# Kernel tuning notes

Measured on AMD Instinct MI355X. Metric: run time of the kernel, lower is better.

The kernel has to match this reference:

```python
import jax, jax.numpy as jnp
import numpy as np

N_NODES = 75000
N_EDGES = 1200000


def gcn_conv(x, src, dst, W, b, n):
    # linear transform first (PyG GCNConv applies lin before propagate)
    h = x @ W  # [n, out]
    # add self loops
    loop = jnp.arange(n, dtype=src.dtype)
    s = jnp.concatenate([src, loop])
    d = jnp.concatenate([dst, loop])
    # symmetric normalization: deg computed on destination after self-loops
    deg = jnp.zeros((n,), dtype=h.dtype).at[d].add(1.0)
    dinv = jnp.where(deg > 0, jax.lax.rsqrt(deg), 0.0)
    norm = dinv[s] * dinv[d]  # [E+n]
    msgs = h[s] * norm[:, None]  # gather + scale, [E+n, out]
    out = jax.ops.segment_sum(msgs, d, num_segments=n)  # scatter-add
    return out + b


def setup_inputs() -> dict:
    key = jax.random.key(0)
    ks = jax.random.split(key, 6)
    x = jax.random.normal(ks[0], (N_NODES, 64), dtype=jnp.float32)
    edge_index = jax.random.randint(ks[1], (2, N_EDGES), 0, N_NODES, dtype=jnp.int64)
    # Glorot-ish scaled weights
    W1 = jax.random.normal(ks[2], (64, 64), dtype=jnp.float32) * (1.0 / np.sqrt(64))
    b1 = jax.random.normal(ks[3], (64,), dtype=jnp.float32) * 0.01
    W2 = jax.random.normal(ks[4], (64, 16), dtype=jnp.float32) * (1.0 / np.sqrt(64))
    b2 = jax.random.normal(ks[5], (16,), dtype=jnp.float32) * 0.01
    return {"x": x, "edge_index": edge_index, "W1": W1, "b1": b1, "W2": W2, "b2": b2}


def reference(x, edge_index, W1, b1, W2, b2):
    src, dst = edge_index[0], edge_index[1]
    h = gcn_conv(x, src, dst, W1, b1, N_NODES)
    h = jax.nn.relu(h)
    # dropout is identity in eval mode
    out = gcn_conv(h, src, dst, W2, b2, N_NODES)
    return out
```

## Files before the change

kernel.cpp:

```cpp
#include <hip/hip_runtime.h>


#define NBSHIFT 9
#define BUCKET_NODES 512
#define CAP 10240
#define CHA 8192
#define TA 512
#define TB 512
#define MAXNB 160
#define EPT 16

__device__ __forceinline__ unsigned bfpack(float a, float b) {
  unsigned ua = __float_as_uint(a), ub = __float_as_uint(b);
  ua += 0x7fffu + ((ua >> 16) & 1u);
  ub += 0x7fffu + ((ub >> 16) & 1u);
  return (ua >> 16) | (ub & 0xffff0000u);
}
__device__ __forceinline__ float bflo(unsigned u) { return __uint_as_float(u << 16); }
__device__ __forceinline__ float bfhi(unsigned u) { return __uint_as_float(u & 0xffff0000u); }

__launch_bounds__(TA)
__global__ void kA_bucket(const int* __restrict__ src, const int* __restrict__ dst,
                          int* __restrict__ bucketCur, int* __restrict__ bucketArr,
                          int NB, int E) {
  __shared__ int stage[CHA];
  __shared__ unsigned char binOf[CHA];
  __shared__ int cnt[MAXNB];
  __shared__ int off[MAXNB];
  __shared__ int gpos[MAXNB];
  __shared__ int cursor[MAXNB];
  __shared__ int scanbuf[256];
  int t = threadIdx.x;
  int e0 = blockIdx.x * CHA;

  for (int i = t; i < NB; i += TA) cnt[i] = 0;
  __syncthreads();
  int dreg[EPT];
  #pragma unroll
  for (int j = 0; j < EPT; j++) {
    int e = e0 + t + j * TA;
    dreg[j] = (e < E) ? dst[e] : -1;
    if (dreg[j] >= 0) atomicAdd(&cnt[dreg[j] >> NBSHIFT], 1);
  }
  __syncthreads();
  if (t < 256) scanbuf[t] = (t < NB) ? cnt[t] : 0;
  __syncthreads();
  for (int o = 1; o < 256; o <<= 1) {
    int add = (t < 256 && t >= o) ? scanbuf[t - o] : 0;
    __syncthreads();
    if (t < 256) scanbuf[t] += add;
    __syncthreads();
  }
  if (t < NB) {
    off[t] = scanbuf[t] - cnt[t];
    cursor[t] = off[t];
    gpos[t] = (cnt[t] > 0) ? atomicAdd(&bucketCur[t], cnt[t]) : 0;
  }
  __syncthreads();
  #pragma unroll
  for (int j = 0; j < EPT; j++) {
    int e = e0 + t + j * TA;
    if (dreg[j] >= 0) {
      int d = dreg[j], s = src[e];
      int b = d >> NBSHIFT;
      int p = atomicAdd(&cursor[b], 1);
      stage[p] = (s << NBSHIFT) | (d & (BUCKET_NODES - 1));
      binOf[p] = (unsigned char)b;
    }
  }
  __syncthreads();
  int total = scanbuf[255];
  for (int i = t; i < total; i += TA) {
    int b = binOf[i];
    int destIdx = gpos[b] + (i - off[b]);
    if (destIdx < CAP) bucketArr[b * CAP + destIdx] = stage[i];
  }
}

__launch_bounds__(TB)
__global__ void kB_fill(const int* __restrict__ bucketArr, const int* __restrict__ bucketCur,
                        int* __restrict__ rp, float* __restrict__ dinv,
                        int* __restrict__ col, int N, int NB) {
  __shared__ int cnts[MAXNB];
  __shared__ int hist[BUCKET_NODES];
  __shared__ int cur[BUCKET_NODES];
  __shared__ int wsum[8], woff[8];
  __shared__ int s_base;
  int b = blockIdx.x;
  int t = threadIdx.x;
  int nE = min(bucketCur[b], CAP);
  int base = b * CAP;

  if (t < NB) cnts[t] = min(bucketCur[t], CAP);
  hist[t] = 0;
  __syncthreads();
  for (int i = t; i < nE; i += TB)
    atomicAdd(&hist[bucketArr[base + i] & (BUCKET_NODES - 1)], 1);
  __syncthreads();
  int myv = hist[t];
  int lane = t & 63, w = t >> 6;
  int incl = myv;
  #pragma unroll
  for (int o = 1; o < 64; o <<= 1) {
    int v = __shfl_up(incl, o);
    if (lane >= o) incl += v;
  }
  if (lane == 63) wsum[w] = incl;
  __syncthreads();
  if (t == 0) {
    int acc = 0;
    for (int i = 0; i < b; i++) acc += cnts[i];
    s_base = acc;
    int a2 = 0;
    #pragma unroll
    for (int i = 0; i < 8; i++) { woff[i] = a2; a2 += wsum[i]; }
    if (b == NB - 1) rp[N] = acc + nE;
  }
  __syncthreads();
  int gexcl = s_base + woff[w] + (incl - myv);
  cur[t] = gexcl;
  int gnode = b * BUCKET_NODES + t;
  if (gnode < N) {
    rp[gnode] = gexcl;
    dinv[gnode] = rsqrtf((float)(myv + 1));
  }
  __syncthreads();
  for (int i = t; i < nE; i += TB) {
    int v = bucketArr[base + i];
    int p = atomicAdd(&cur[v & (BUCKET_NODES - 1)], 1);
    col[p] = v >> NBSHIFT;
  }
}

__launch_bounds__(256)
__global__ void k_gemm64(const float4* __restrict__ X4, const float4* __restrict__ W4,
                         const float* __restrict__ dinv, uint2* __restrict__ outb,
                         int n) {
  __shared__ float4 Xs[64 * 17];
  __shared__ float4 Ws[64 * 16];
  int t = threadIdx.x;
  int base = blockIdx.x * 64;
  {
    int rr = t >> 2, q = t & 3;
    int r = base + rr;
    #pragma unroll
    for (int c = 0; c < 4; c++) {
      float4 v = make_float4(0.f, 0.f, 0.f, 0.f);
      if (r < n) v = X4[r * 16 + q * 4 + c];
      Xs[rr * 17 + q * 4 + c] = v;
      Ws[t + 256 * c] = W4[t + 256 * c];
    }
  }
  __syncthreads();

  int tx = t & 15, ty = t >> 4;
  float4 a0 = make_float4(0.f, 0.f, 0.f, 0.f), a1 = a0, a2 = a0, a3 = a0;
  #pragma unroll
  for (int kb = 0; kb < 16; kb++) {
    float4 x0 = Xs[(ty * 4 + 0) * 17 + kb];
    float4 x1 = Xs[(ty * 4 + 1) * 17 + kb];
    float4 x2 = Xs[(ty * 4 + 2) * 17 + kb];
    float4 x3 = Xs[(ty * 4 + 3) * 17 + kb];
    float4 w0 = Ws[(kb * 4 + 0) * 16 + tx];
    float4 w1 = Ws[(kb * 4 + 1) * 16 + tx];
    float4 w2 = Ws[(kb * 4 + 2) * 16 + tx];
    float4 w3 = Ws[(kb * 4 + 3) * 16 + tx];
    #define FMA4(A, XS) \
      A.x = fmaf(XS.x, w0.x, A.x); A.y = fmaf(XS.x, w0.y, A.y); \
      A.z = fmaf(XS.x, w0.z, A.z); A.w = fmaf(XS.x, w0.w, A.w); \
      A.x = fmaf(XS.y, w1.x, A.x); A.y = fmaf(XS.y, w1.y, A.y); \
      A.z = fmaf(XS.y, w1.z, A.z); A.w = fmaf(XS.y, w1.w, A.w); \
      A.x = fmaf(XS.z, w2.x, A.x); A.y = fmaf(XS.z, w2.y, A.y); \
      A.z = fmaf(XS.z, w2.z, A.z); A.w = fmaf(XS.z, w2.w, A.w); \
      A.x = fmaf(XS.w, w3.x, A.x); A.y = fmaf(XS.w, w3.y, A.y); \
      A.z = fmaf(XS.w, w3.z, A.z); A.w = fmaf(XS.w, w3.w, A.w);
    FMA4(a0, x0) FMA4(a1, x1) FMA4(a2, x2) FMA4(a3, x3)
    #undef FMA4
  }
  #pragma unroll
  for (int i = 0; i < 4; i++) {
    int r = base + ty * 4 + i;
    if (r < n) {
      float s = dinv[r];
      float4 a = (i == 0) ? a0 : (i == 1) ? a1 : (i == 2) ? a2 : a3;
      uint2 pk;
      pk.x = bfpack(a.x * s, a.y * s);
      pk.y = bfpack(a.z * s, a.w * s);
      outb[r * 16 + tx] = pk;
    }
  }
}

__launch_bounds__(256)
__global__ void k_aggW2(const uint2* __restrict__ hsb,
                        const int* __restrict__ rp,
                        const int* __restrict__ col,
                        const float* __restrict__ dinv,
                        const float* __restrict__ b1,
                        const float* __restrict__ W2,
                        unsigned* __restrict__ hs2b,
                        int n) {
  __shared__ float W2s[1024];
  for (int i = threadIdx.x; i < 1024; i += 256) W2s[i] = W2[i];
  __syncthreads();
  int lane = threadIdx.x & 63;
  int c = lane & 15;
  int node = ((blockIdx.x * blockDim.x + threadIdx.x) >> 6) * 4 + (lane >> 4);
  if (node >= n) return;

  float4 b14 = ((const float4*)b1)[c];
  int s0 = rp[node], s1 = rp[node + 1];
  int dt = s1 - s0 + 1;
  float ax = 0.f, ay = 0.f, az = 0.f, aw = 0.f;
  int t = 0;
  int i0 = node, i1 = 0, i2 = 0, i3 = 0, i4 = 0, i5 = 0, i6 = 0, i7 = 0;
  if (1 < dt) i1 = col[s0 + 0];
  if (2 < dt) i2 = col[s0 + 1];
  if (3 < dt) i3 = col[s0 + 2];
  if (4 < dt) i4 = col[s0 + 3];
  if (5 < dt) i5 = col[s0 + 4];
  if (6 < dt) i6 = col[s0 + 5];
  if (7 < dt) i7 = col[s0 + 6];
  while (t < dt) {
    int c0 = i0, c1 = i1, c2 = i2, c3 = i3, c4 = i4, c5 = i5, c6 = i6, c7 = i7;
    bool h1_ = (t + 1) < dt, h2_ = (t + 2) < dt, h3_ = (t + 3) < dt;
    bool h4_ = (t + 4) < dt, h5_ = (t + 5) < dt, h6_ = (t + 6) < dt;
    bool h7_ = (t + 7) < dt;
    int tn = t + 8;
    if (tn + 0 < dt) i0 = col[s0 + tn - 1];
    if (tn + 1 < dt) i1 = col[s0 + tn + 0];
    if (tn + 2 < dt) i2 = col[s0 + tn + 1];
    if (tn + 3 < dt) i3 = col[s0 + tn + 2];
    if (tn + 4 < dt) i4 = col[s0 + tn + 3];
    if (tn + 5 < dt) i5 = col[s0 + tn + 4];
    if (tn + 6 < dt) i6 = col[s0 + tn + 5];
    if (tn + 7 < dt) i7 = col[s0 + tn + 6];
    uint2 u0 = hsb[c0 * 16 + c];
    uint2 u1 = h1_ ? hsb[c1 * 16 + c] : make_uint2(0u, 0u);
    uint2 u2 = h2_ ? hsb[c2 * 16 + c] : make_uint2(0u, 0u);
    uint2 u3 = h3_ ? hsb[c3 * 16 + c] : make_uint2(0u, 0u);
    uint2 u4 = h4_ ? hsb[c4 * 16 + c] : make_uint2(0u, 0u);
    uint2 u5 = h5_ ? hsb[c5 * 16 + c] : make_uint2(0u, 0u);
    uint2 u6 = h6_ ? hsb[c6 * 16 + c] : make_uint2(0u, 0u);
    uint2 u7 = h7_ ? hsb[c7 * 16 + c] : make_uint2(0u, 0u);
    #define ACC(U) \
      ax += bflo(U.x); ay += bfhi(U.x); az += bflo(U.y); aw += bfhi(U.y);
    ACC(u0) ACC(u1) ACC(u2) ACC(u3) ACC(u4) ACC(u5) ACC(u6) ACC(u7)
    #undef ACC
    t = tn;
  }
  float dv = dinv[node];
  float h0  = fmaxf(ax * dv + b14.x, 0.f);
  float h1v = fmaxf(ay * dv + b14.y, 0.f);
  float h2v = fmaxf(az * dv + b14.z, 0.f);
  float h3v = fmaxf(aw * dv + b14.w, 0.f);

  float val = 0.f;
  int gb = lane & 48;
  #pragma unroll
  for (int kq = 0; kq < 16; kq++) {
    int srcl = gb + kq;
    float v0 = __shfl(h0, srcl);
    float v1 = __shfl(h1v, srcl);
    float v2 = __shfl(h2v, srcl);
    float v3 = __shfl(h3v, srcl);
    val = fmaf(v0, W2s[(4 * kq + 0) * 16 + c], val);
    val = fmaf(v1, W2s[(4 * kq + 1) * 16 + c], val);
    val = fmaf(v2, W2s[(4 * kq + 2) * 16 + c], val);
    val = fmaf(v3, W2s[(4 * kq + 3) * 16 + c], val);
  }
  val *= dv;
  float vnext = __shfl_down(val, 1);
  if ((c & 1) == 0) hs2b[node * 8 + (c >> 1)] = bfpack(val, vnext);
}

__launch_bounds__(256)
__global__ void k_agg16(const uint2* __restrict__ hs2b,
                        const int* __restrict__ rp,
                        const int* __restrict__ col,
                        const float* __restrict__ dinv,
                        const float* __restrict__ b2,
                        float4* __restrict__ out4,
                        int n) {
  int lane = threadIdx.x & 63;
  int hl = lane & 7;
  int c = hl & 3;
  int sub = hl >> 2;
  int node = ((blockIdx.x * blockDim.x + threadIdx.x) >> 6) * 8 + (lane >> 3);
  if (node >= n) return;

  int s0 = rp[node], s1 = rp[node + 1];
  int dt = s1 - s0 + 1;
  float ax = 0.f, ay = 0.f, az = 0.f, aw = 0.f;
  int t = sub;
  int i0 = 0, i1 = 0, i2 = 0, i3 = 0;
  if (t < dt)     i0 = (t == 0) ? node : col[s0 + t - 1];
  if (t + 2 < dt) i1 = col[s0 + t + 1];
  if (t + 4 < dt) i2 = col[s0 + t + 3];
  if (t + 6 < dt) i3 = col[s0 + t + 5];
  while (t < dt) {
    int c0 = i0, c1 = i1, c2 = i2, c3 = i3;
    bool h1_ = (t + 2) < dt, h2_ = (t + 4) < dt, h3_ = (t + 6) < dt;
    int tn = t + 8;
    if (tn < dt)     i0 = col[s0 + tn - 1];
    if (tn + 2 < dt) i1 = col[s0 + tn + 1];
    if (tn + 4 < dt) i2 = col[s0 + tn + 3];
    if (tn + 6 < dt) i3 = col[s0 + tn + 5];
    uint2 u0 = hs2b[c0 * 4 + c];
    uint2 u1 = h1_ ? hs2b[c1 * 4 + c] : make_uint2(0u, 0u);
    uint2 u2 = h2_ ? hs2b[c2 * 4 + c] : make_uint2(0u, 0u);
    uint2 u3 = h3_ ? hs2b[c3 * 4 + c] : make_uint2(0u, 0u);
    ax += bflo(u0.x) + bflo(u1.x) + bflo(u2.x) + bflo(u3.x);
    ay += bfhi(u0.x) + bfhi(u1.x) + bfhi(u2.x) + bfhi(u3.x);
    az += bflo(u0.y) + bflo(u1.y) + bflo(u2.y) + bflo(u3.y);
    aw += bfhi(u0.y) + bfhi(u1.y) + bfhi(u2.y) + bfhi(u3.y);
    t = tn;
  }
  ax += __shfl_xor(ax, 4);
  ay += __shfl_xor(ay, 4);
  az += __shfl_xor(az, 4);
  aw += __shfl_xor(aw, 4);
  if (sub == 0) {
    float dv = dinv[node];
    float4 b24 = ((const float4*)b2)[c];
    float4 o;
    o.x = ax * dv + b24.x;
    o.y = ay * dv + b24.y;
    o.z = az * dv + b24.z;
    o.w = aw * dv + b24.w;
    out4[node * 4 + c] = o;
  }
}

extern "C" void kernel_launch(void* const* d_in, const int* in_sizes, int n_in,
                              void* d_out, int out_size, void* d_ws, size_t ws_size,
                              hipStream_t stream) {
  const float* x  = (const float*)d_in[0];
  const int* edges = (const int*)d_in[1];
  const float* W1 = (const float*)d_in[2];
  const float* b1 = (const float*)d_in[3];
  const float* W2 = (const float*)d_in[4];
  const float* b2 = (const float*)d_in[5];
  float* out = (float*)d_out;

  const int N = in_sizes[0] / 64;
  const int E = in_sizes[1] / 2;
  const int* src = edges;
  const int* dst = edges + E;
  const int NB = (N + BUCKET_NODES - 1) >> NBSHIFT;

  auto align = [](size_t v) { return (v + 255) & ~(size_t)255; };
  char* p = (char*)d_ws;
  float* dinv       = (float*)p; p += align((size_t)N * 4);
  int*   rp         = (int*)p;   p += align((size_t)(N + 1) * 4);
  int*   bucketCur  = (int*)p;   p += align((size_t)MAXNB * 4);
  int*   col        = (int*)p;   p += align((size_t)E * 4);
  float* hs1        = (float*)p; p += align((size_t)N * 64 * 4);
  float* hs2        = (float*)p; p += align((size_t)N * 16 * 2);
  int* bucketArr = (int*)hs1;

  const int nbA = (E + CHA - 1) / CHA;
  const int nbW4 = (int)((((size_t)(N + 3) / 4) * 64 + 255) / 256);
  const int nbW8 = (int)((((size_t)(N + 7) / 8) * 64 + 255) / 256);

  hipMemsetAsync(bucketCur, 0, (size_t)MAXNB * 4, stream);
  kA_bucket<<<nbA, TA, 0, stream>>>(src, dst, bucketCur, bucketArr, NB, E);
  kB_fill  <<<NB, TB, 0, stream>>>(bucketArr, bucketCur, rp, dinv, col, N, NB);

  k_gemm64<<<(N + 63) / 64, 256, 0, stream>>>((const float4*)x, (const float4*)W1,
                                              dinv, (uint2*)hs1, N);
  k_aggW2 <<<nbW4, 256, 0, stream>>>((const uint2*)hs1, rp, col, dinv,
                                     b1, W2, (unsigned*)hs2, N);
  k_agg16 <<<nbW8, 256, 0, stream>>>((const uint2*)hs2, rp, col, dinv,
                                     b2, (float4*)out, N);
}
```

Measured before the change: 117.2 us.

## Replace global atomic bucket cursors with per-block fixed-slot segments

The bucketing pass now writes each block's edges into a fixed-capacity slot per (bucket, block) pair and records the per-block counts, instead of reserving space with global atomics. This removes the memset and the contended atomicAdd on the bucket cursors. The fill kernel sums the counts, compacts the segments into shared memory and then builds the CSR as before. The cost is extra count reduction work in every fill block and a larger scratch footprint. Edges beyond the per-block slot cap are dropped, and at about 51 expected edges per slot overflow is unlikely but not guarded. The scratch layout also reuses the hs1 region, which now has to be big enough for both uses.

```diff
diff --git a/kernel.cpp b/kernel.cpp
--- a/kernel.cpp
+++ b/kernel.cpp
@@ -8,6 +8,7 @@
 #define TA 512
 #define TB 512
 #define MAXNB 160
+#define SCAP 128
 #define EPT 16
 
 __device__ __forceinline__ unsigned bfpack(float a, float b) {
@@ -21,17 +22,18 @@
 
 __launch_bounds__(TA)
 __global__ void kA_bucket(const int* __restrict__ src, const int* __restrict__ dst,
-                          int* __restrict__ bucketCur, int* __restrict__ bucketArr,
-                          int NB, int E) {
+                          int* __restrict__ bucketCnt,
+                          int* __restrict__ bucketArr,
+                          int NB, int nbA, int E) {
   __shared__ int stage[CHA];
   __shared__ unsigned char binOf[CHA];
   __shared__ int cnt[MAXNB];
   __shared__ int off[MAXNB];
-  __shared__ int gpos[MAXNB];
   __shared__ int cursor[MAXNB];
   __shared__ int scanbuf[256];
   int t = threadIdx.x;
-  int e0 = blockIdx.x * CHA;
+  int blk = blockIdx.x;
+  int e0 = blk * CHA;
 
   for (int i = t; i < NB; i += TA) cnt[i] = 0;
   __syncthreads();
@@ -54,7 +56,7 @@
   if (t < NB) {
     off[t] = scanbuf[t] - cnt[t];
     cursor[t] = off[t];
-    gpos[t] = (cnt[t] > 0) ? atomicAdd(&bucketCur[t], cnt[t]) : 0;
+    bucketCnt[blk * MAXNB + t] = min(cnt[t], SCAP);
   }
   __syncthreads();
   #pragma unroll
@@ -72,30 +74,58 @@
   int total = scanbuf[255];
   for (int i = t; i < total; i += TA) {
     int b = binOf[i];
-    int destIdx = gpos[b] + (i - off[b]);
-    if (destIdx < CAP) bucketArr[b * CAP + destIdx] = stage[i];
+    int j = i - off[b];
+    if (j < SCAP)
+      bucketArr[((size_t)b * nbA + blk) * SCAP + j] = stage[i];
   }
 }
 
 __launch_bounds__(TB)
-__global__ void kB_fill(const int* __restrict__ bucketArr, const int* __restrict__ bucketCur,
+__global__ void kB_fill(const int* __restrict__ bucketArr,
+                        const int* __restrict__ bucketCnt,
                         int* __restrict__ rp, float* __restrict__ dinv,
-                        int* __restrict__ col, int N, int NB) {
-  __shared__ int cnts[MAXNB];
+                        int* __restrict__ col, int N, int NB, int nbA) {
+  __shared__ int segLen[MAXNB];
+  __shared__ int segBase[MAXNB];
+  __shared__ int tot[MAXNB];
+  __shared__ int stagingE[CAP];
   __shared__ int hist[BUCKET_NODES];
   __shared__ int cur[BUCKET_NODES];
   __shared__ int wsum[8], woff[8];
-  __shared__ int s_base;
+  __shared__ int s_base, s_nE;
   int b = blockIdx.x;
   int t = threadIdx.x;
-  int nE = min(bucketCur[b], CAP);
-  int base = b * CAP;
-
-  if (t < NB) cnts[t] = min(bucketCur[t], CAP);
+
+  if (t < NB) {
+    int acc = 0;
+    for (int blk = 0; blk < nbA; blk++) acc += bucketCnt[blk * MAXNB + t];
+    tot[t] = acc;
+  }
+  if (t < nbA) segLen[t] = bucketCnt[t * MAXNB + b];
+  __syncthreads();
+  if (t == 0) {
+    int acc = 0;
+    for (int i = 0; i < b; i++) acc += tot[i];
+    s_base = acc;
+    int sb = 0;
+    for (int i = 0; i < nbA; i++) { segBase[i] = sb; sb += segLen[i]; }
+    s_nE = sb;
+    if (b == NB - 1) rp[N] = acc + sb;
+  }
+  __syncthreads();
+  int nE = s_nE;
+  int iters = (nbA * SCAP + TB - 1) / TB;
+  for (int it = 0; it < iters; it++) {
+    int idx = it * TB + t;
+    int blk = idx >> 7;
+    int j = idx & (SCAP - 1);
+    if (blk < nbA && j < segLen[blk])
+      stagingE[segBase[blk] + j] = bucketArr[((size_t)b * nbA + blk) * SCAP + j];
+  }
   hist[t] = 0;
   __syncthreads();
   for (int i = t; i < nE; i += TB)
-    atomicAdd(&hist[bucketArr[base + i] & (BUCKET_NODES - 1)], 1);
+    atomicAdd(&hist[stagingE[i] & (BUCKET_NODES - 1)], 1);
   __syncthreads();
   int myv = hist[t];
   int lane = t & 63, w = t >> 6;
@@ -108,13 +138,9 @@
   if (lane == 63) wsum[w] = incl;
   __syncthreads();
   if (t == 0) {
-    int acc = 0;
-    for (int i = 0; i < b; i++) acc += cnts[i];
-    s_base = acc;
     int a2 = 0;
     #pragma unroll
     for (int i = 0; i < 8; i++) { woff[i] = a2; a2 += wsum[i]; }
-    if (b == NB - 1) rp[N] = acc + nE;
   }
   __syncthreads();
   int gexcl = s_base + woff[w] + (incl - myv);
@@ -126,7 +152,7 @@
   }
   __syncthreads();
   for (int i = t; i < nE; i += TB) {
-    int v = bucketArr[base + i];
+    int v = stagingE[i];
     int p = atomicAdd(&cur[v & (BUCKET_NODES - 1)], 1);
     col[p] = v >> NBSHIFT;
   }
@@ -348,24 +374,23 @@
   const int* src = edges;
   const int* dst = edges + E;
   const int NB = (N + BUCKET_NODES - 1) >> NBSHIFT;
+  const int nbA = (E + CHA - 1) / CHA;
 
   auto align = [](size_t v) { return (v + 255) & ~(size_t)255; };
   char* p = (char*)d_ws;
   float* dinv       = (float*)p; p += align((size_t)N * 4);
   int*   rp         = (int*)p;   p += align((size_t)(N + 1) * 4);
-  int*   bucketCur  = (int*)p;   p += align((size_t)MAXNB * 4);
+  int*   bucketCnt  = (int*)p;   p += align((size_t)MAXNB * MAXNB * 4);
   int*   col        = (int*)p;   p += align((size_t)E * 4);
-  float* hs1        = (float*)p; p += align((size_t)N * 64 * 4);
+  float* hs1        = (float*)p; p += align((size_t)MAXNB * MAXNB * SCAP * 4);
   float* hs2        = (float*)p; p += align((size_t)N * 16 * 2);
   int* bucketArr = (int*)hs1;
 
-  const int nbA = (E + CHA - 1) / CHA;
   const int nbW4 = (int)((((size_t)(N + 3) / 4) * 64 + 255) / 256);
   const int nbW8 = (int)((((size_t)(N + 7) / 8) * 64 + 255) / 256);
 
-  hipMemsetAsync(bucketCur, 0, (size_t)MAXNB * 4, stream);
-  kA_bucket<<<nbA, TA, 0, stream>>>(src, dst, bucketCur, bucketArr, NB, E);
-  kB_fill  <<<NB, TB, 0, stream>>>(bucketArr, bucketCur, rp, dinv, col, N, NB);
+  kA_bucket<<<nbA, TA, 0, stream>>>(src, dst, bucketCnt, bucketArr, NB, nbA, E);
+  kB_fill  <<<NB, TB, 0, stream>>>(bucketArr, bucketCnt, rp, dinv, col, N, NB, nbA);
 
   k_gemm64<<<(N + 63) / 64, 256, 0, stream>>>((const float4*)x, (const float4*)W1,
                                               dinv, (uint2*)hs1, N);
```

Measured after the change: 138.9 us. +18.5%, slower.
